# Kernel tuning notes

Hardware: AMD Instinct MI355X
Metric: run time of the kernel (lower is better)

Reference implementation:

```python
import jax, jax.numpy as jnp
import numpy as np

D_MODEL = 1024
NUM_HEADS = 16
HEAD_DIM = D_MODEL // NUM_HEADS  # 64
ROT_DIM = 32
WINDOW = 512
ROT_BASE = 10000.0
B, L = 4, 2048


def _rotary_cos_sin(Lq, dtype):
    inv_freq = 1.0 / ROT_BASE ** (jnp.arange(0, ROT_DIM, 2, dtype=jnp.float32) / ROT_DIM)
    t = jnp.arange(Lq, dtype=jnp.float32)
    freqs = jnp.outer(t, inv_freq)  # (L, ROT_DIM//2)
    return jnp.cos(freqs).astype(dtype), jnp.sin(freqs).astype(dtype)


def _apply_rotary(x, cos, sin):
    # x: (B, H, L, Dh); rotate first ROT_DIM dims, NeoX (non-interleaved) style
    x_ro, x_rest = x[..., :ROT_DIM], x[..., ROT_DIM:]
    x1, x2 = jnp.split(x_ro, 2, axis=-1)
    c = cos[None, None, :, :]
    s = sin[None, None, :, :]
    xr = jnp.concatenate([x1 * c - x2 * s, x2 * c + x1 * s], axis=-1)
    return jnp.concatenate([xr, x_rest], axis=-1)


def setup_inputs() -> dict:
    key = jax.random.key(0)
    k1, k2, k3 = jax.random.split(key, 3)
    x = jax.random.normal(k1, (B, L, D_MODEL), dtype=jnp.float32)
    attn_mask = jnp.ones((B, L), dtype=jnp.bool_)
    Wqkv_kernel = jax.random.normal(k2, (D_MODEL, 3 * D_MODEL), dtype=jnp.float32) * (D_MODEL ** -0.5)
    out_proj_kernel = jax.random.normal(k3, (D_MODEL, D_MODEL), dtype=jnp.float32) * (D_MODEL ** -0.5)
    return {"x": x, "attn_mask": attn_mask, "Wqkv_kernel": Wqkv_kernel, "out_proj_kernel": out_proj_kernel}


def reference(x, attn_mask, Wqkv_kernel, out_proj_kernel):
    Bx, Lx, _ = x.shape
    qkv = jnp.einsum('bld,de->ble', x, Wqkv_kernel)  # (B, L, 3*D)
    q, k, v = jnp.split(qkv, 3, axis=-1)

    def split_heads(t):
        return t.reshape(Bx, Lx, NUM_HEADS, HEAD_DIM).transpose(0, 2, 1, 3)

    q, k, v = split_heads(q), split_heads(k), split_heads(v)
    cos, sin = _rotary_cos_sin(Lx, q.dtype)
    q = _apply_rotary(q, cos, sin)
    k = _apply_rotary(k, cos, sin)

    scale = HEAD_DIM ** (-0.5)
    scores = jnp.einsum('bhqd,bhkd->bhqk', q, k) * scale  # (B, H, L, L)
    idx = jnp.arange(Lx)
    causal = idx[None, :] > idx[:, None]  # key > query -> mask
    win = idx[None, :] < idx[:, None] - (WINDOW - 1)  # too far in the past -> mask
    pad = ~attn_mask[:, None, None, :]  # (B,1,1,L) padded keys -> mask
    neg = -jnp.inf
    scores = jnp.where(causal[None, None] | win[None, None] | pad, neg, scores)
    attn = jax.nn.softmax(scores, axis=-1)
    ctx = jnp.einsum('bhqk,bhkd->bhqd', attn, v)
    ctx = ctx.transpose(0, 2, 1, 3).reshape(Bx, Lx, D_MODEL)
    out = jnp.einsum('bld,de->ble', ctx, out_proj_kernel)
    return out
```

## Files before the change

### kernel.cpp

```cpp
#include <hip/hip_runtime.h>
#include <hip/hip_bf16.h>
#include <stdint.h>

#define B_    4
#define L_    2048
#define H_    16
#define DH_   64
#define DM_   1024
#define M_    8192
#define WIN_  512

typedef short  short8 __attribute__((ext_vector_type(8)));
typedef __bf16 bf16x8 __attribute__((ext_vector_type(8)));
typedef float  f32x4  __attribute__((ext_vector_type(4)));
typedef unsigned short us4 __attribute__((ext_vector_type(4)));

__device__ __forceinline__ unsigned short f2bf(float f) {
  return __builtin_bit_cast(unsigned short, __float2bfloat16(f));
}
__device__ __forceinline__ f32x4 mfma16(short8 a, short8 b, f32x4 c) {
  return __builtin_amdgcn_mfma_f32_16x16x32_bf16(
      __builtin_bit_cast(bf16x8, a), __builtin_bit_cast(bf16x8, b), c, 0, 0, 0);
}
__device__ __forceinline__ void async16(const void* g, void* lds) {
  __builtin_amdgcn_global_load_lds(
      (const __attribute__((address_space(1))) void*)g,
      (__attribute__((address_space(3))) void*)lds, 16, 0, 0);
}
template<int N> __device__ __forceinline__ void vmwait() {
  if constexpr (N == 4)      asm volatile("s_waitcnt vmcnt(4)" ::: "memory");
  else                       asm volatile("s_waitcnt vmcnt(0)" ::: "memory");
}

__global__ __launch_bounds__(256) void k_cvt(const float* __restrict__ in,
                                             unsigned short* __restrict__ out, int n) {
  int idx = (blockIdx.x * 256 + threadIdx.x) * 4;
  if (idx >= n) return;
  float4 f = *(const float4*)(in + idx);
  us4 o;
  o[0] = f2bf(f.x); o[1] = f2bf(f.y); o[2] = f2bf(f.z); o[3] = f2bf(f.w);
  *(us4*)(out + idx) = o;
}

__global__ __launch_bounds__(256) void k_wt(const float* __restrict__ W,
                                            unsigned short* __restrict__ WT, int N_) {
  __shared__ unsigned short t[32][33];
  int n0 = blockIdx.x * 32, k0 = blockIdx.y * 32;
  int tid = threadIdx.x;
  int r = tid >> 3, c4 = (tid & 7) * 4;
  float4 f = *(const float4*)(W + (size_t)(k0 + r) * N_ + n0 + c4);
  t[r][c4 + 0] = f2bf(f.x); t[r][c4 + 1] = f2bf(f.y);
  t[r][c4 + 2] = f2bf(f.z); t[r][c4 + 3] = f2bf(f.w);
  __syncthreads();
  unsigned short* dst = WT + (size_t)(n0 + r) * 1024 + k0 + c4;
  dst[0] = t[c4 + 0][r]; dst[1] = t[c4 + 1][r];
  dst[2] = t[c4 + 2][r]; dst[3] = t[c4 + 3][r];
}

__global__ __launch_bounds__(256) void k_rope(float* __restrict__ C, float* __restrict__ S) {
  int idx = blockIdx.x * 256 + threadIdx.x;
  int tpos = idx >> 4, fi = idx & 15;
  float freq = 1.0f / powf(10000.0f, (float)fi / 16.0f);
  float a = (float)tpos * freq;
  C[idx] = cosf(a);
  S[idx] = sinf(a);
}

__device__ __forceinline__ void gemm128(const unsigned short* __restrict__ A,
                                        const unsigned short* __restrict__ Bt,
                                        int m0, int n0, unsigned short* lds,
                                        f32x4 (&acc)[4][4]) {
  constexpr int SLOT = 8192;
  const int tid = threadIdx.x, lane = tid & 63;
  const int wave = tid >> 6, wn = wave & 1, wm = wave >> 1;
  const int llo = lane & 15, lhi = lane >> 4;
  const int swz = (llo >> 1) & 3;
  const int rbase = wm * 64, cbase = wn * 64;

  auto stage = [&](int t) {
    unsigned short* s = lds + (t % 3) * SLOT;
    const int kt = t * 32;
#pragma unroll
    for (int i = 0; i < 2; ++i) {
      int q = i * 256 + tid;
      int row = q >> 2, cs = (q & 3) ^ ((row >> 1) & 3);
      async16(A + (size_t)(m0 + row) * DM_ + kt + cs * 8, s + q * 8);
    }
#pragma unroll
    for (int i = 0; i < 2; ++i) {
      int q = i * 256 + tid;
      int row = q >> 2, cs = (q & 3) ^ ((row >> 1) & 3);
      async16(Bt + (size_t)(n0 + row) * DM_ + kt + cs * 8, s + 4096 + q * 8);
    }
  };

  stage(0); stage(1);
#pragma unroll 4
  for (int t = 0; t < 32; ++t) {
    if (t < 31) vmwait<4>(); else vmwait<0>();
    __builtin_amdgcn_s_barrier();
    if (t + 2 < 32) stage(t + 2);
    const unsigned short* sa = lds + (t % 3) * SLOT;
    const unsigned short* sb = sa + 4096;
    short8 af[4], bf[4];
#pragma unroll
    for (int i = 0; i < 4; ++i)
      af[i] = *(const short8*)(sa + (rbase + i * 16 + llo) * 32 + ((lhi ^ swz) << 3));
#pragma unroll
    for (int j = 0; j < 4; ++j)
      bf[j] = *(const short8*)(sb + (cbase + j * 16 + llo) * 32 + ((lhi ^ swz) << 3));
    __builtin_amdgcn_s_setprio(1);
#pragma unroll
    for (int i = 0; i < 4; ++i)
#pragma unroll
      for (int j = 0; j < 4; ++j)
        acc[i][j] = mfma16(af[i], bf[j], acc[i][j]);
    __builtin_amdgcn_s_setprio(0);
  }
}

__global__ __launch_bounds__(256, 3) void k_gemm_qkv(const unsigned short* __restrict__ X,
                                                     const unsigned short* __restrict__ WT,
                                                     unsigned short* __restrict__ Q,
                                                     unsigned short* __restrict__ Kq,
                                                     unsigned short* __restrict__ V,
                                                     const float* __restrict__ COS,
                                                     const float* __restrict__ SIN) {
  __shared__ unsigned short lds[3 * 8192];
  const int wgid = blockIdx.x;
  const int m0 = (wgid & 63) * 128, n0 = (wgid >> 6) * 128;
  f32x4 acc[4][4];
#pragma unroll
  for (int i = 0; i < 4; ++i)
#pragma unroll
    for (int j = 0; j < 4; ++j) acc[i][j] = f32x4{0.f, 0.f, 0.f, 0.f};

  gemm128(X, WT, m0, n0, lds, acc);

  const int tid = threadIdx.x, lane = tid & 63;
  const int wave = tid >> 6, wn = wave & 1, wm = wave >> 1;
  const int llo = lane & 15, lhi = lane >> 4;
  const int ncol = n0 + wn * 64;
  const int sec = ncol >> 10;
  const int h = (ncol & 1023) >> 6;
  unsigned short* dst = (sec == 0) ? Q : (sec == 1 ? Kq : V);
  const bool rot = (sec < 2);
  const float qs = (sec == 0) ? 0.18033688f : 1.0f;
#pragma unroll
  for (int i = 0; i < 4; ++i) {
#pragma unroll
    for (int r = 0; r < 4; ++r) {
      int m = m0 + wm * 64 + i * 16 + lhi * 4 + r;
      int b = m >> 11, l = m & 2047;
      float c0 = acc[i][0][r], c1 = acc[i][1][r];
      float c2 = acc[i][2][r], c3 = acc[i][3][r];
      if (rot) {
        float cs = COS[l * 16 + llo], sn = SIN[l * 16 + llo];
        float n0v = c0 * cs - c1 * sn;
        float n1v = c1 * cs + c0 * sn;
        c0 = n0v; c1 = n1v;
      }
      c0 *= qs; c1 *= qs; c2 *= qs; c3 *= qs;
      size_t base = ((size_t)(b * H_ + h) * L_ + l) * DH_;
      dst[base +      llo] = f2bf(c0);
      dst[base + 16 + llo] = f2bf(c1);
      dst[base + 32 + llo] = f2bf(c2);
      dst[base + 48 + llo] = f2bf(c3);
    }
  }
}

__global__ __launch_bounds__(256, 3) void k_gemm_out(const unsigned short* __restrict__ A,
                                                     const unsigned short* __restrict__ WT,
                                                     float* __restrict__ Cout) {
  __shared__ unsigned short lds[3 * 8192];
  const int wgid = blockIdx.x;
  const int m0 = (wgid & 63) * 128, n0 = (wgid >> 6) * 128;
  f32x4 acc[4][4];
#pragma unroll
  for (int i = 0; i < 4; ++i)
#pragma unroll
    for (int j = 0; j < 4; ++j) acc[i][j] = f32x4{0.f, 0.f, 0.f, 0.f};

  gemm128(A, WT, m0, n0, lds, acc);

  const int tid = threadIdx.x, lane = tid & 63;
  const int wave = tid >> 6, wn = wave & 1, wm = wave >> 1;
  const int llo = lane & 15, lhi = lane >> 4;
#pragma unroll
  for (int i = 0; i < 4; ++i)
#pragma unroll
    for (int r = 0; r < 4; ++r) {
      int m = m0 + wm * 64 + i * 16 + lhi * 4 + r;
#pragma unroll
      for (int j = 0; j < 4; ++j)
        Cout[(size_t)m * DM_ + n0 + wn * 64 + j * 16 + llo] = acc[i][j][r];
    }
}

__global__ __launch_bounds__(256) void k_vt(const unsigned short* __restrict__ V,
                                            unsigned short* __restrict__ VT) {
  __shared__ unsigned short t[64][65];
  int l0 = blockIdx.x * 64, bh = blockIdx.y;
  int tid = threadIdx.x;
  int r = tid >> 2, c = (tid & 3) * 16;
  const unsigned short* src = V + ((size_t)bh * L_ + l0 + r) * DH_ + c;
#pragma unroll
  for (int k = 0; k < 16; ++k) t[r][c + k] = src[k];
  __syncthreads();
  unsigned short* dst = VT + ((size_t)bh * DH_ + r) * L_ + l0 + c;
#pragma unroll
  for (int k = 0; k < 16; ++k) dst[k] = t[c + k][r];
}

__global__ __launch_bounds__(256) __attribute__((amdgpu_waves_per_eu(3, 4)))
void k_attn(const unsigned short* __restrict__ Q,
            const unsigned short* __restrict__ Kg,
            const unsigned short* __restrict__ VT,
            unsigned short* __restrict__ CTX) {
  __shared__ unsigned short lk[2][4096];
  __shared__ unsigned short lv[2][4096];
  __shared__ unsigned short lp[4][2048];
  const int tid = threadIdx.x, wave = tid >> 6, lane = tid & 63;
  const int bh = blockIdx.x;
  const int qs = 15 - blockIdx.y;
  const int q0 = qs * 128, wq0 = q0 + wave * 32;
  const int llo = lane & 15, lhi = lane >> 4;
  const int psw = llo & 7;

  short8 qa[2][2];
#pragma unroll
  for (int f = 0; f < 2; ++f) {
    const short8* qp = (const short8*)(Q + ((size_t)bh * L_ + wq0 + f * 16 + llo) * DH_ + lhi * 8);
    qa[f][0] = qp[0];
    qa[f][1] = qp[4];
  }

  f32x4 ctxa[2][4];
#pragma unroll
  for (int f = 0; f < 2; ++f)
#pragma unroll
    for (int j = 0; j < 4; ++j) ctxa[f][j] = f32x4{0.f, 0.f, 0.f, 0.f};
  float m_q[2] = {-1e30f, -1e30f};
  float l_q[2] = {0.f, 0.f};

  const int t0b = (q0 > (WIN_ - 1) ? q0 - (WIN_ - 1) : 0) >> 6;
  const int t1b = (q0 + 127) >> 6;
  char* lpw = (char*)lp[wave];

  auto stage = [&](int buf, int t) {
    const int k0s = t * 64;
#pragma unroll
    for (int i = 0; i < 2; ++i) {
      int g = i * 256 + tid;
      int row = g >> 3;
      int cs = (g & 7) ^ (row & 7);
      async16(Kg + ((size_t)bh * L_ + k0s + row) * DH_ + cs * 8, &lk[buf][g * 8]);
      async16(VT + ((size_t)bh * DH_ + row) * L_ + k0s + cs * 8, &lv[buf][g * 8]);
    }
  };

  stage(0, t0b);
  __syncthreads();
  int cur = 0;

  for (int t = t0b; t <= t1b; ++t) {
    if (t < t1b) stage(cur ^ 1, t + 1);
    const int k0 = t * 64;

    if (!(k0 > wq0 + 31 || k0 + 63 < wq0 - (WIN_ - 1))) {
      const unsigned short* lkc = lk[cur];
      const unsigned short* lvc = lv[cur];
      const bool interior = (k0 + 63 <= wq0) && (k0 >= wq0 - (WIN_ - 32));

#pragma unroll
      for (int f = 0; f < 2; ++f) {
        f32x4 s[4];
        __builtin_amdgcn_s_setprio(1);
#pragma unroll
        for (int j = 0; j < 4; ++j) {
          int row = j * 16 + llo;
          short8 kb0 = *(const short8*)&lkc[row * 64 + ((lhi ^ psw) << 3)];
          short8 kb1 = *(const short8*)&lkc[row * 64 + (((lhi + 4) ^ psw) << 3)];
          s[j] = mfma16(kb0, qa[f][0], f32x4{0.f, 0.f, 0.f, 0.f});
          s[j] = mfma16(kb1, qa[f][1], s[j]);
        }
        __builtin_amdgcn_s_setprio(0);

        const int q = wq0 + f * 16 + llo;
        if (!interior) {
#pragma unroll
          for (int j = 0; j < 4; ++j)
#pragma unroll
            for (int r = 0; r < 4; ++r) {
              int key = k0 + j * 16 + lhi * 4 + r;
              s[j][r] = (key <= q && key >= q - (WIN_ - 1)) ? s[j][r] : -1e30f;
            }
        }
        float mj0 = fmaxf(fmaxf(s[0][0], s[0][1]), fmaxf(s[0][2], s[0][3]));
        float mj1 = fmaxf(fmaxf(s[1][0], s[1][1]), fmaxf(s[1][2], s[1][3]));
        float mj2 = fmaxf(fmaxf(s[2][0], s[2][1]), fmaxf(s[2][2], s[2][3]));
        float mj3 = fmaxf(fmaxf(s[3][0], s[3][1]), fmaxf(s[3][2], s[3][3]));
        float lmax = fmaxf(fmaxf(mj0, mj1), fmaxf(mj2, mj3));

        if (!__all(lmax <= m_q[f] + 11.0f)) {
          float m1 = lmax;
          m1 = fmaxf(m1, __shfl_xor(m1, 16));
          m1 = fmaxf(m1, __shfl_xor(m1, 32));
          float mnew = fmaxf(m_q[f], m1);
          float alpha = __builtin_amdgcn_exp2f(m_q[f] - mnew);
          m_q[f] = mnew;
          l_q[f] *= alpha;
#pragma unroll
          for (int r = 0; r < 4; ++r) {
            float ar = __shfl(alpha, (lane & 48) | (lhi * 4 + r));
#pragma unroll
            for (int j = 0; j < 4; ++j) ctxa[f][j][r] *= ar;
          }
        }

        char* rowb = lpw + (f * 16 + llo) * 128;
        float lacc = 0.f;
#pragma unroll
        for (int j = 0; j < 4; ++j) {
          float p0 = __builtin_amdgcn_exp2f(s[j][0] - m_q[f]);
          float p1 = __builtin_amdgcn_exp2f(s[j][1] - m_q[f]);
          float p2 = __builtin_amdgcn_exp2f(s[j][2] - m_q[f]);
          float p3 = __builtin_amdgcn_exp2f(s[j][3] - m_q[f]);
          lacc += (p0 + p1) + (p2 + p3);
          us4 pk;
          pk[0] = f2bf(p0); pk[1] = f2bf(p1); pk[2] = f2bf(p2); pk[3] = f2bf(p3);
          int swc = (2 * j + (lhi >> 1)) ^ psw;
          *(us4*)(rowb + swc * 16 + (lhi & 1) * 8) = pk;
        }
        l_q[f] += lacc;
      }

      short8 pa[2][2];
#pragma unroll
      for (int f = 0; f < 2; ++f) {
        char* rowb = lpw + (f * 16 + llo) * 128;
        pa[f][0] = *(const short8*)(rowb + ((lhi ^ psw) << 4));
        pa[f][1] = *(const short8*)(rowb + (((lhi + 4) ^ psw) << 4));
      }
      __builtin_amdgcn_s_setprio(1);
#pragma unroll
      for (int j = 0; j < 4; ++j) {
        int row = j * 16 + llo;
        short8 vb0 = *(const short8*)&lvc[row * 64 + ((lhi ^ psw) << 3)];
        short8 vb1 = *(const short8*)&lvc[row * 64 + (((lhi + 4) ^ psw) << 3)];
        ctxa[0][j] = mfma16(pa[0][0], vb0, ctxa[0][j]);
        ctxa[0][j] = mfma16(pa[0][1], vb1, ctxa[0][j]);
        ctxa[1][j] = mfma16(pa[1][0], vb0, ctxa[1][j]);
        ctxa[1][j] = mfma16(pa[1][1], vb1, ctxa[1][j]);
      }
      __builtin_amdgcn_s_setprio(0);
    }

    __syncthreads();
    cur ^= 1;
  }

  const int b = bh >> 4, h = bh & 15;
#pragma unroll
  for (int f = 0; f < 2; ++f) {
    float lt = l_q[f];
    lt += __shfl_xor(lt, 16);
    lt += __shfl_xor(lt, 32);
    float li = 1.0f / lt;
#pragma unroll
    for (int r = 0; r < 4; ++r) {
      float linv = __shfl(li, (lane & 48) | (lhi * 4 + r));
      int qrow = wq0 + f * 16 + lhi * 4 + r;
      size_t base = ((size_t)b * L_ + qrow) * DM_ + h * DH_;
#pragma unroll
      for (int j = 0; j < 4; ++j)
        __builtin_nontemporal_store(f2bf(ctxa[f][j][r] * linv), &CTX[base + j * 16 + llo]);
    }
  }
}

extern "C" void kernel_launch(void* const* d_in, const int* in_sizes, int n_in,
                              void* d_out, int out_size, void* d_ws, size_t ws_size,
                              hipStream_t stream) {
  (void)in_sizes; (void)n_in; (void)out_size; (void)ws_size;
  const float* x    = (const float*)d_in[0];
  const float* wqkv = (const float*)d_in[2];
  const float* wout = (const float*)d_in[3];
  float* out = (float*)d_out;

  char* w = (char*)d_ws;
  unsigned short* X   = (unsigned short*)(w);
  unsigned short* WQT = (unsigned short*)(w + 16777216);
  unsigned short* POT = (unsigned short*)(w + 23068672);
  float*          COS = (float*)(w + 25165824);
  float*          SIN = (float*)(w + 25296896);
  unsigned short* Qb  = (unsigned short*)(w + 25427968);
  unsigned short* Kb  = (unsigned short*)(w + 25427968 + 16777216);
  unsigned short* Vb  = (unsigned short*)(w + 25427968 + 2*16777216);
  unsigned short* VTb = (unsigned short*)(w + 25427968 + 3*16777216);
  unsigned short* CTX = X;

  k_cvt<<<dim3(8192), dim3(256), 0, stream>>>(x, X, M_ * DM_);
  k_wt<<<dim3(96, 32), dim3(256), 0, stream>>>(wqkv, WQT, 3072);
  k_wt<<<dim3(32, 32), dim3(256), 0, stream>>>(wout, POT, 1024);
  k_rope<<<dim3(128), dim3(256), 0, stream>>>(COS, SIN);
  k_gemm_qkv<<<dim3(1536), dim3(256), 0, stream>>>(X, WQT, Qb, Kb, Vb, COS, SIN);
  k_vt<<<dim3(32, 64), dim3(256), 0, stream>>>(Vb, VTb);
  k_attn<<<dim3(64, 16), dim3(256), 0, stream>>>(Qb, Kb, VTb, CTX);
  k_gemm_out<<<dim3(512), dim3(256), 0, stream>>>(CTX, POT, out);
}
```

Baseline: 156.7 us.

## Enlarge GEMM tiles to 256x128 with 8 waves and 64-wide K steps

Both projection GEMMs now use 512-thread workgroups computing 256x128 output tiles with a K step of 64, a triple-buffered 48KB-per-slot LDS pipeline, and an XOR swizzle over 8 chunks. Prefetches of the next-next stage are split across two sub-steps, with barriers around the MFMA blocks. The larger tiles are meant to reuse B across more rows and halve the number of K iterations and barriers. In exchange LDS per block grows to 144KB, which limits occupancy, and the extra barriers per iteration add synchronization.

New measurement: 160.8 us, median of 2. +2.6%, slower.

```diff
diff --git a/kernel.cpp b/kernel.cpp
--- a/kernel.cpp
+++ b/kernel.cpp
@@ -28,7 +28,8 @@
       (__attribute__((address_space(3))) void*)lds, 16, 0, 0);
 }
 template<int N> __device__ __forceinline__ void vmwait() {
-  if constexpr (N == 4)      asm volatile("s_waitcnt vmcnt(4)" ::: "memory");
+  if constexpr (N == 6)      asm volatile("s_waitcnt vmcnt(6)" ::: "memory");
+  else if constexpr (N == 4) asm volatile("s_waitcnt vmcnt(4)" ::: "memory");
   else                       asm volatile("s_waitcnt vmcnt(0)" ::: "memory");
 }
 
@@ -66,76 +67,93 @@
   S[idx] = sinf(a);
 }
 
-__device__ __forceinline__ void gemm128(const unsigned short* __restrict__ A,
+__device__ __forceinline__ void gemm_dp(const unsigned short* __restrict__ A,
                                         const unsigned short* __restrict__ Bt,
                                         int m0, int n0, unsigned short* lds,
                                         f32x4 (&acc)[4][4]) {
-  constexpr int SLOT = 8192;
+  constexpr int SLOT = 24576;
   const int tid = threadIdx.x, lane = tid & 63;
   const int wave = tid >> 6, wn = wave & 1, wm = wave >> 1;
   const int llo = lane & 15, lhi = lane >> 4;
-  const int swz = (llo >> 1) & 3;
+  const int psw = llo & 7;
   const int rbase = wm * 64, cbase = wn * 64;
 
-  auto stage = [&](int t) {
+  auto stageA = [&](int t, int half) {
     unsigned short* s = lds + (t % 3) * SLOT;
-    const int kt = t * 32;
+    const int kt = t * 64;
+#pragma unroll
+    for (int i = half * 2; i < half * 2 + 2; ++i) {
+      int q = i * 512 + tid;
+      int row = q >> 3, cs = (q & 7) ^ (row & 7);
+      async16(A + (size_t)(m0 + row) * DM_ + kt + cs * 8, s + q * 8);
+    }
+  };
+  auto stageB = [&](int t) {
+    unsigned short* s = lds + (t % 3) * SLOT + 16384;
+    const int kt = t * 64;
 #pragma unroll
     for (int i = 0; i < 2; ++i) {
-      int q = i * 256 + tid;
-      int row = q >> 2, cs = (q & 3) ^ ((row >> 1) & 3);
-      async16(A + (size_t)(m0 + row) * DM_ + kt + cs * 8, s + q * 8);
-    }
-#pragma unroll
-    for (int i = 0; i < 2; ++i) {
-      int q = i * 256 + tid;
-      int row = q >> 2, cs = (q & 3) ^ ((row >> 1) & 3);
-      async16(Bt + (size_t)(n0 + row) * DM_ + kt + cs * 8, s + 4096 + q * 8);
+      int q = i * 512 + tid;
+      int row = q >> 3, cs = (q & 7) ^ (row & 7);
+      async16(Bt + (size_t)(n0 + row) * DM_ + kt + cs * 8, s + q * 8);
     }
   };
 
-  stage(0); stage(1);
-#pragma unroll 4
-  for (int t = 0; t < 32; ++t) {
-    if (t < 31) vmwait<4>(); else vmwait<0>();
-    __builtin_amdgcn_s_barrier();
-    if (t + 2 < 32) stage(t + 2);
+  stageA(0, 0); stageA(0, 1); stageB(0);
+  stageA(1, 0); stageA(1, 1); stageB(1);
+  vmwait<6>();
+  __builtin_amdgcn_s_barrier();
+
+  for (int t = 0; t < 16; ++t) {
     const unsigned short* sa = lds + (t % 3) * SLOT;
-    const unsigned short* sb = sa + 4096;
-    short8 af[4], bf[4];
-#pragma unroll
-    for (int i = 0; i < 4; ++i)
-      af[i] = *(const short8*)(sa + (rbase + i * 16 + llo) * 32 + ((lhi ^ swz) << 3));
-#pragma unroll
-    for (int j = 0; j < 4; ++j)
-      bf[j] = *(const short8*)(sb + (cbase + j * 16 + llo) * 32 + ((lhi ^ swz) << 3));
-    __builtin_amdgcn_s_setprio(1);
-#pragma unroll
-    for (int i = 0; i < 4; ++i)
-#pragma unroll
-      for (int j = 0; j < 4; ++j)
-        acc[i][j] = mfma16(af[i], bf[j], acc[i][j]);
-    __builtin_amdgcn_s_setprio(0);
+    const unsigned short* sb = sa + 16384;
+    const bool pre = (t + 2 < 16);
+#define RD_A(i, kk) (*(const short8*)(sa + (rbase + (i)*16 + llo) * 64 + (((lhi) + (kk)*4) ^ psw) * 8))
+#define RD_B(j, kk) (*(const short8*)(sb + (cbase + (j)*16 + llo) * 64 + (((lhi) + (kk)*4) ^ psw) * 8))
+#pragma unroll
+    for (int kk = 0; kk < 2; ++kk) {
+      short8 af[4], bf[4];
+      af[0] = RD_A(0, kk); af[1] = RD_A(1, kk); af[2] = RD_A(2, kk); af[3] = RD_A(3, kk);
+      bf[0] = RD_B(0, kk); bf[1] = RD_B(1, kk); bf[2] = RD_B(2, kk); bf[3] = RD_B(3, kk);
+      if (pre) {
+        if (kk == 0) { stageA(t + 2, 0); stageA(t + 2, 1); }
+        else         { stageB(t + 2); }
+      }
+      asm volatile("" ::: "memory");
+      __builtin_amdgcn_s_barrier();
+      __builtin_amdgcn_s_setprio(1);
+#pragma unroll
+      for (int i = 0; i < 4; ++i)
+#pragma unroll
+        for (int j = 0; j < 4; ++j)
+          acc[i][j] = mfma16(af[i], bf[j], acc[i][j]);
+      __builtin_amdgcn_s_setprio(0);
+      if (kk == 1) { if (t < 14) vmwait<6>(); else vmwait<0>(); }
+      asm volatile("" ::: "memory");
+      __builtin_amdgcn_s_barrier();
+    }
+#undef RD_A
+#undef RD_B
   }
 }
 
-__global__ __launch_bounds__(256, 3) void k_gemm_qkv(const unsigned short* __restrict__ X,
+__global__ __launch_bounds__(512, 2) void k_gemm_qkv(const unsigned short* __restrict__ X,
                                                      const unsigned short* __restrict__ WT,
                                                      unsigned short* __restrict__ Q,
                                                      unsigned short* __restrict__ Kq,
                                                      unsigned short* __restrict__ V,
                                                      const float* __restrict__ COS,
                                                      const float* __restrict__ SIN) {
-  __shared__ unsigned short lds[3 * 8192];
+  __shared__ unsigned short lds[3 * 24576];
   const int wgid = blockIdx.x;
-  const int m0 = (wgid & 63) * 128, n0 = (wgid >> 6) * 128;
+  const int m0 = (wgid & 31) * 256, n0 = (wgid >> 5) * 128;
   f32x4 acc[4][4];
 #pragma unroll
   for (int i = 0; i < 4; ++i)
 #pragma unroll
     for (int j = 0; j < 4; ++j) acc[i][j] = f32x4{0.f, 0.f, 0.f, 0.f};
 
-  gemm128(X, WT, m0, n0, lds, acc);
+  gemm_dp(X, WT, m0, n0, lds, acc);
 
   const int tid = threadIdx.x, lane = tid & 63;
   const int wave = tid >> 6, wn = wave & 1, wm = wave >> 1;
@@ -170,19 +188,19 @@
   }
 }
 
-__global__ __launch_bounds__(256, 3) void k_gemm_out(const unsigned short* __restrict__ A,
+__global__ __launch_bounds__(512, 2) void k_gemm_out(const unsigned short* __restrict__ A,
                                                      const unsigned short* __restrict__ WT,
                                                      float* __restrict__ Cout) {
-  __shared__ unsigned short lds[3 * 8192];
+  __shared__ unsigned short lds[3 * 24576];
   const int wgid = blockIdx.x;
-  const int m0 = (wgid & 63) * 128, n0 = (wgid >> 6) * 128;
+  const int m0 = (wgid & 31) * 256, n0 = (wgid >> 5) * 128;
   f32x4 acc[4][4];
 #pragma unroll
   for (int i = 0; i < 4; ++i)
 #pragma unroll
     for (int j = 0; j < 4; ++j) acc[i][j] = f32x4{0.f, 0.f, 0.f, 0.f};
 
-  gemm128(A, WT, m0, n0, lds, acc);
+  gemm_dp(A, WT, m0, n0, lds, acc);
 
   const int tid = threadIdx.x, lane = tid & 63;
   const int wave = tid >> 6, wn = wave & 1, wm = wave >> 1;
@@ -405,8 +423,8 @@
   k_wt<<<dim3(96, 32), dim3(256), 0, stream>>>(wqkv, WQT, 3072);
   k_wt<<<dim3(32, 32), dim3(256), 0, stream>>>(wout, POT, 1024);
   k_rope<<<dim3(128), dim3(256), 0, stream>>>(COS, SIN);
-  k_gemm_qkv<<<dim3(1536), dim3(256), 0, stream>>>(X, WQT, Qb, Kb, Vb, COS, SIN);
+  k_gemm_qkv<<<dim3(768), dim3(512), 0, stream>>>(X, WQT, Qb, Kb, Vb, COS, SIN);
   k_vt<<<dim3(32, 64), dim3(256), 0, stream>>>(Vb, VTb);
   k_attn<<<dim3(64, 16), dim3(256), 0, stream>>>(Qb, Kb, VTb, CTX);
-  k_gemm_out<<<dim3(512), dim3(256), 0, stream>>>(CTX, POT, out);
-}
+  k_gemm_out<<<dim3(256), dim3(512), 0, stream>>>(CTX, POT, out);
+}
```

## Fuse V transpose into QKV GEMM epilogue via LDS-staged vectorized stores

Applied to the files above, without the earlier changes.

The QKV GEMM epilogue now stages each wave's 64x64 output tile in shared memory and writes it out with 16-byte vector stores, instead of scattered 2-byte stores. V tiles are written transposed directly into the VT layout, so the separate k_vt kernel launch and its extra V buffer round trip are removed. This adds a barrier and LDS traffic to the epilogue and reuses the GEMM's LDS buffer after the main loop.

New measurement: 149.7 us. -4.5%, faster.

```diff
diff --git a/kernel.cpp b/kernel.cpp
--- a/kernel.cpp
+++ b/kernel.cpp
@@ -123,7 +123,7 @@
                                                      const unsigned short* __restrict__ WT,
                                                      unsigned short* __restrict__ Q,
                                                      unsigned short* __restrict__ Kq,
-                                                     unsigned short* __restrict__ V,
+                                                     unsigned short* __restrict__ VT,
                                                      const float* __restrict__ COS,
                                                      const float* __restrict__ SIN) {
   __shared__ unsigned short lds[3 * 8192];
@@ -143,29 +143,55 @@
   const int ncol = n0 + wn * 64;
   const int sec = ncol >> 10;
   const int h = (ncol & 1023) >> 6;
-  unsigned short* dst = (sec == 0) ? Q : (sec == 1 ? Kq : V);
   const bool rot = (sec < 2);
   const float qs = (sec == 0) ? 0.18033688f : 1.0f;
+
+  __syncthreads();
+  unsigned short* lw = lds + wave * 4608;
+
 #pragma unroll
   for (int i = 0; i < 4; ++i) {
 #pragma unroll
     for (int r = 0; r < 4; ++r) {
       int m = m0 + wm * 64 + i * 16 + lhi * 4 + r;
-      int b = m >> 11, l = m & 2047;
+      int l = m & 2047;
       float c0 = acc[i][0][r], c1 = acc[i][1][r];
       float c2 = acc[i][2][r], c3 = acc[i][3][r];
       if (rot) {
         float cs = COS[l * 16 + llo], sn = SIN[l * 16 + llo];
         float n0v = c0 * cs - c1 * sn;
         float n1v = c1 * cs + c0 * sn;
-        c0 = n0v; c1 = n1v;
+        c0 = n0v * qs; c1 = n1v * qs; c2 *= qs; c3 *= qs;
+        unsigned short* rw = lw + (i * 16 + lhi * 4 + r) * 72;
+        rw[llo] = f2bf(c0); rw[16 + llo] = f2bf(c1);
+        rw[32 + llo] = f2bf(c2); rw[48 + llo] = f2bf(c3);
+      } else {
+        int col = i * 16 + lhi * 4 + r;
+        lw[llo * 72 + col]        = f2bf(c0);
+        lw[(16 + llo) * 72 + col] = f2bf(c1);
+        lw[(32 + llo) * 72 + col] = f2bf(c2);
+        lw[(48 + llo) * 72 + col] = f2bf(c3);
       }
-      c0 *= qs; c1 *= qs; c2 *= qs; c3 *= qs;
-      size_t base = ((size_t)(b * H_ + h) * L_ + l) * DH_;
-      dst[base +      llo] = f2bf(c0);
-      dst[base + 16 + llo] = f2bf(c1);
-      dst[base + 32 + llo] = f2bf(c2);
-      dst[base + 48 + llo] = f2bf(c3);
+    }
+  }
+  const int mb = m0 + wm * 64;
+  const int b = mb >> 11, l0 = mb & 2047;
+  if (sec < 2) {
+    unsigned short* dst = (sec == 0) ? Q : Kq;
+#pragma unroll
+    for (int it = 0; it < 8; ++it) {
+      int row = it * 8 + (lane >> 3);
+      int ch = lane & 7;
+      short8 v = *(const short8*)(lw + row * 72 + ch * 8);
+      *(short8*)(dst + ((size_t)(b * H_ + h) * L_ + l0 + row) * DH_ + ch * 8) = v;
+    }
+  } else {
+#pragma unroll
+    for (int it = 0; it < 8; ++it) {
+      int d = it * 8 + (lane >> 3);
+      int ch = lane & 7;
+      short8 v = *(const short8*)(lw + d * 72 + ch * 8);
+      *(short8*)(VT + ((size_t)(b * H_ + h) * DH_ + d) * L_ + l0 + ch * 8) = v;
     }
   }
 }
@@ -196,21 +222,6 @@
       for (int j = 0; j < 4; ++j)
         Cout[(size_t)m * DM_ + n0 + wn * 64 + j * 16 + llo] = acc[i][j][r];
     }
-}
-
-__global__ __launch_bounds__(256) void k_vt(const unsigned short* __restrict__ V,
-                                            unsigned short* __restrict__ VT) {
-  __shared__ unsigned short t[64][65];
-  int l0 = blockIdx.x * 64, bh = blockIdx.y;
-  int tid = threadIdx.x;
-  int r = tid >> 2, c = (tid & 3) * 16;
-  const unsigned short* src = V + ((size_t)bh * L_ + l0 + r) * DH_ + c;
-#pragma unroll
-  for (int k = 0; k < 16; ++k) t[r][c + k] = src[k];
-  __syncthreads();
-  unsigned short* dst = VT + ((size_t)bh * DH_ + r) * L_ + l0 + c;
-#pragma unroll
-  for (int k = 0; k < 16; ++k) dst[k] = t[c + k][r];
 }
 
 __global__ __launch_bounds__(256) __attribute__((amdgpu_waves_per_eu(3, 4)))
@@ -397,16 +408,14 @@
   float*          SIN = (float*)(w + 25296896);
   unsigned short* Qb  = (unsigned short*)(w + 25427968);
   unsigned short* Kb  = (unsigned short*)(w + 25427968 + 16777216);
-  unsigned short* Vb  = (unsigned short*)(w + 25427968 + 2*16777216);
-  unsigned short* VTb = (unsigned short*)(w + 25427968 + 3*16777216);
+  unsigned short* VTb = (unsigned short*)(w + 25427968 + 2*16777216);
   unsigned short* CTX = X;
 
   k_cvt<<<dim3(8192), dim3(256), 0, stream>>>(x, X, M_ * DM_);
   k_wt<<<dim3(96, 32), dim3(256), 0, stream>>>(wqkv, WQT, 3072);
   k_wt<<<dim3(32, 32), dim3(256), 0, stream>>>(wout, POT, 1024);
   k_rope<<<dim3(128), dim3(256), 0, stream>>>(COS, SIN);
-  k_gemm_qkv<<<dim3(1536), dim3(256), 0, stream>>>(X, WQT, Qb, Kb, Vb, COS, SIN);
-  k_vt<<<dim3(32, 64), dim3(256), 0, stream>>>(Vb, VTb);
+  k_gemm_qkv<<<dim3(1536), dim3(256), 0, stream>>>(X, WQT, Qb, Kb, VTb, COS, SIN);
   k_attn<<<dim3(64, 16), dim3(256), 0, stream>>>(Qb, Kb, VTb, CTX);
   k_gemm_out<<<dim3(512), dim3(256), 0, stream>>>(CTX, POT, out);
 }
```
